# Performance work log

Hardware: AMD Instinct MI355X
Metric: run time of the kernel (lower is better)

## Reference

```python
import jax, jax.numpy as jnp
import numpy as np

EMBED_DIM = 1024
NUM_HEADS = 16
HEAD_WIDTH = 64  # EMBED_DIM == NUM_HEADS * HEAD_WIDTH
B, L = 2, 1024


def setup_inputs() -> dict:
    key = jax.random.key(0)
    ks = jax.random.split(key, 7)
    s = EMBED_DIM ** -0.5
    return {
        "x": jax.random.normal(ks[0], (B, L, EMBED_DIM), dtype=jnp.float32),
        "bias": jax.random.normal(ks[1], (B, L, L, NUM_HEADS), dtype=jnp.float32),
        # nn.Linear weights are (out_features, in_features)
        "w_proj": jax.random.normal(ks[2], (3 * EMBED_DIM, EMBED_DIM), dtype=jnp.float32) * s,
        "w_o": jax.random.normal(ks[3], (EMBED_DIM, EMBED_DIM), dtype=jnp.float32) * s,
        "b_o": jnp.zeros((EMBED_DIM,), dtype=jnp.float32),
        "w_g": jax.random.normal(ks[4], (EMBED_DIM, EMBED_DIM), dtype=jnp.float32) * s,
        "b_g": jnp.ones((EMBED_DIM,), dtype=jnp.float32),
    }


def reference(x, bias, w_proj, w_o, b_o, w_g, b_g):
    b, l, e = x.shape
    h, hw = NUM_HEADS, HEAD_WIDTH
    # fused QKV projection: (B,L,3E) -> (B,H,L,3*hw), head-major split as in torch
    t = jnp.einsum('ble,fe->blf', x, w_proj)
    t = t.reshape(b, l, h, 3 * hw).transpose(0, 2, 1, 3)  # (B,H,L,3hw)
    q, k, v = jnp.split(t, 3, axis=-1)
    q = q * (hw ** -0.5)
    a = jnp.einsum('bhqc,bhkc->bhqk', q, k)
    a = a + bias.transpose(0, 3, 1, 2)  # bias: (B,Lq,Lk,H) -> (B,H,Lq,Lk)
    a = jax.nn.softmax(a, axis=-1)
    y = jnp.einsum('bhqk,bhkc->bqhc', a, v).reshape(b, l, e)
    g = jax.nn.sigmoid(jnp.einsum('ble,fe->blf', x, w_g) + b_g)
    y = g * y
    y = jnp.einsum('ble,fe->blf', y, w_o) + b_o
    # faithful to original rearrange('... lq lk h -> ... h lq lk') applied to (B,h,lq,lk):
    attn = jnp.transpose(a, (0, 3, 1, 2))  # (B, lk, h, lq)
    return y, attn
```

## Files before the change

kernel.cpp:

```cpp
#include <hip/hip_runtime.h>
#include <hip/hip_bf16.h>
#include <stdint.h>

typedef __attribute__((ext_vector_type(4))) float f32x4;
typedef __attribute__((ext_vector_type(8))) short short8;
typedef __attribute__((ext_vector_type(4))) unsigned short u16x4;
typedef unsigned short us;

#define DEV __device__ __forceinline__
#define MFMA16(a, b, c) __builtin_amdgcn_mfma_f32_16x16x32_bf16(a, b, c, 0, 0, 0)

DEV us f2b(float x) {
  union { float f; uint32_t u; } c; c.f = x;
  uint32_t r = (c.u + 0x7fffu + ((c.u >> 16) & 1u)) >> 16;
  return (us)r;
}
DEV float b2f(us x) {
  union { uint32_t u; float f; } c; c.u = ((uint32_t)x) << 16;
  return c.f;
}

DEV void gload_lds16(const void* g, void* l) {
  __builtin_amdgcn_global_load_lds((const __attribute__((address_space(1))) void*)g,
                                   (__attribute__((address_space(3))) void*)l, 16, 0, 0);
}

__global__ __launch_bounds__(256) void prep_k(
    const float* __restrict__ x, const float* __restrict__ wproj,
    const float* __restrict__ wg, const float* __restrict__ wo,
    us* __restrict__ Xbf, us* __restrict__ Wbf, us* __restrict__ Wobf) {
  int i = blockIdx.x * 256 + threadIdx.x;
  const float* src; us* dst;
  if (i < 524288)               { src = x     + (size_t)i * 4;                  dst = Xbf + (size_t)i * 4; }
  else if (i < 524288 + 786432) { int j = i - 524288;            src = wproj + (size_t)j * 4; dst = Wbf + (size_t)j * 4; }
  else if (i < 524288 + 786432 + 262144) { int j = i - (524288 + 786432); src = wg + (size_t)j * 4; dst = Wbf + 3145728 + (size_t)j * 4; }
  else                          { int j = i - (524288 + 786432 + 262144); src = wo + (size_t)j * 4; dst = Wobf + (size_t)j * 4; }
  f32x4 v = *(const f32x4*)src;
  u16x4 o; o.x = f2b(v.x); o.y = f2b(v.y); o.z = f2b(v.z); o.w = f2b(v.w);
  *(u16x4*)dst = o;
}

DEV void gemm_stage(char* sm, const us* A, const us* Bw,
                    int tileMrow, int tileNrow, int buf, int kt, int lane, int wid) {
  const char* gA = (const char*)A;
  const char* gB = (const char*)Bw;
#pragma unroll
  for (int i = 0; i < 2; ++i) {
    int c = wid * 2 + i;
    int off = c * 1024 + lane * 16;
    int r = off >> 6, cb = off & 63;
    gload_lds16(gA + ((size_t)(tileMrow + r) * 2048) + kt * 64 + cb, sm + buf * 8192 + c * 1024);
    gload_lds16(gB + ((size_t)(tileNrow + r) * 2048) + kt * 64 + cb, sm + 16384 + buf * 8192 + c * 1024);
  }
}

DEV void gemm_main(const us* A, const us* Bw,
                   int tileMrow, int tileNrow, f32x4 acc[4][4], char* sm) {
  int tid = threadIdx.x, lane = tid & 63, wid = tid >> 6;
  int wr = wid >> 1, wc = wid & 1;
  gemm_stage(sm, A, Bw, tileMrow, tileNrow, 0, 0, lane, wid);
  for (int kt = 0; kt < 32; ++kt) {
    __syncthreads();
    if (kt < 31) gemm_stage(sm, A, Bw, tileMrow, tileNrow, (kt + 1) & 1, kt + 1, lane, wid);
    int ab = (kt & 1) * 8192;
    int rb = (lane & 15) * 64 + ((lane >> 4) * 16);
    short8 af[4], bf[4];
#pragma unroll
    for (int mi = 0; mi < 4; ++mi)
      af[mi] = *(const short8*)(sm + ab + (wr * 64 + mi * 16) * 64 + rb);
#pragma unroll
    for (int ni = 0; ni < 4; ++ni)
      bf[ni] = *(const short8*)(sm + 16384 + ab + (wc * 64 + ni * 16) * 64 + rb);
#pragma unroll
    for (int mi = 0; mi < 4; ++mi)
#pragma unroll
      for (int ni = 0; ni < 4; ++ni)
        acc[mi][ni] = MFMA16(af[mi], bf[ni], acc[mi][ni]);
  }
}

__global__ __launch_bounds__(256) void gemm_qkvg_k(
    const us* __restrict__ Xbf, const us* __restrict__ Wbf,
    us* __restrict__ Qb, us* __restrict__ Kb, us* __restrict__ Vt,
    float* __restrict__ G, const float* __restrict__ bg) {
  __shared__ char sm[32768];
  int bid = blockIdx.x;
  int swz = (bid & 7) * 64 + (bid >> 3);
  int tileM = swz >> 5, tileN = swz & 31;
  f32x4 acc[4][4] = {};
  gemm_main(Xbf, Wbf, tileM * 128, tileN * 128, acc, sm);
  int lane = threadIdx.x & 63, wid = threadIdx.x >> 6;
  int wr = wid >> 1, wc = wid & 1;
#pragma unroll
  for (int mi = 0; mi < 4; ++mi)
#pragma unroll
    for (int ni = 0; ni < 4; ++ni)
#pragma unroll
      for (int j = 0; j < 4; ++j) {
        int row = tileM * 128 + wr * 64 + mi * 16 + ((lane >> 4) << 2) + j;
        int col = tileN * 128 + wc * 64 + ni * 16 + (lane & 15);
        float v = acc[mi][ni][j];
        int b = row >> 10, l = row & 1023;
        if (col < 3072) {
          int h = col / 192, r = col - h * 192;
          size_t base = ((size_t)(b * 16 + h) * 1024 + l) * 64;
          if (r < 64)        Qb[base + r] = f2b(v * 0.125f);
          else if (r < 128)  Kb[base + (r - 64)] = f2b(v);
          else               Vt[((size_t)(b * 16 + h) * 64 + (r - 128)) * 1024 + l] = f2b(v);
        } else {
          int e = col - 3072;
          float s = v + bg[e];
          G[(size_t)row * 1024 + e] = 1.f / (1.f + __expf(-s));
        }
      }
}

__global__ __launch_bounds__(512, 8) void qke_k(
    const us* __restrict__ Qb, const us* __restrict__ Kb,
    const float* __restrict__ bias, us* __restrict__ E,
    float* __restrict__ lpart) {
  __shared__ float bt[2][8][16][36];
  int tid = threadIdx.x, lane = tid & 63, w = tid >> 6;
  int la = lane & 15, lg = lane >> 4;
  int bid = blockIdx.x;
  int b = (bid & 7) >> 2, kc = bid & 3;
  int hg = (bid >> 3) & 1, qt = bid >> 4;
  int lq0 = qt * 16, lk00 = kc * 256;
  int h = hg * 8 + w;
  int hh = w;

  short8 qf[2];
  {
    size_t bh = (size_t)(b * 16 + h);
#pragma unroll
    for (int ks = 0; ks < 2; ++ks)
      qf[ks] = *(const short8*)(Qb + bh * 65536 + (size_t)(lq0 + la) * 64 + ks * 32 + lg * 8);
  }
  const us* Kh = Kb + (size_t)(b * 16 + h) * 65536;
  const float* bsrc = bias + ((size_t)b << 24) + ((size_t)lq0 << 14) + hg * 8;

#pragma unroll
  for (int i = 0; i < 2; ++i) {
    int f = tid + i * 512;
    int h4 = f & 1, lk = (f >> 1) & 31, q = f >> 6;
    f32x4 v = *(const f32x4*)(bsrc + ((size_t)q << 14) + ((size_t)(lk00 + lk) << 4) + h4 * 4);
#pragma unroll
    for (int e = 0; e < 4; ++e) {
      int hl = h4 * 4 + e;
      bt[0][hl][q][lk ^ (hl << 2)] = v[e];
    }
  }

  float lacc = 0.f;
#pragma unroll 1
  for (int sc = 0; sc < 8; ++sc) {
    __syncthreads();
    if (sc < 7) {
      int lkg2 = lk00 + (sc + 1) * 32;
      int nb = (sc + 1) & 1;
#pragma unroll
      for (int i = 0; i < 2; ++i) {
        int f = tid + i * 512;
        int h4 = f & 1, lk = (f >> 1) & 31, q = f >> 6;
        f32x4 v = *(const f32x4*)(bsrc + ((size_t)q << 14) + ((size_t)(lkg2 + lk) << 4) + h4 * 4);
#pragma unroll
        for (int e = 0; e < 4; ++e) {
          int hl = h4 * 4 + e;
          bt[nb][hl][q][lk ^ (hl << 2)] = v[e];
        }
      }
    }
    int cb = sc & 1;
    int lkg = lk00 + sc * 32;
#pragma unroll
    for (int fr = 0; fr < 2; ++fr) {
      const us* kr = Kh + (size_t)(lkg + fr * 16 + la) * 64 + lg * 8;
      short8 kf0 = *(const short8*)kr;
      short8 kf1 = *(const short8*)(kr + 32);
      int lkb = (fr * 16 + lg * 4) ^ (hh << 2);
      f32x4 a = *(const f32x4*)&bt[cb][hh][la][lkb];
      a = MFMA16(kf0, qf[0], a);
      a = MFMA16(kf1, qf[1], a);
      u16x4 ev;
#pragma unroll
      for (int j = 0; j < 4; ++j) {
        float e = __expf(a[j]);
        lacc += e;
        ev[j] = f2b(e);
      }
      *(u16x4*)(E + (((size_t)(b * 1024 + lq0 + la) * 16 + h) << 10) + lkg + fr * 16 + lg * 4) = ev;
    }
  }
  {
    float s = lacc;
    s += __shfl_xor(s, 16);
    s += __shfl_xor(s, 32);
    if (lg == 0) lpart[kc * 32768 + (b * 16 + h) * 1024 + lq0 + la] = s;
  }
}

__global__ __launch_bounds__(256) void pv_k(
    const us* __restrict__ E, const us* __restrict__ Vt,
    const float* __restrict__ lpart, const float* __restrict__ G,
    float* __restrict__ outa, us* __restrict__ Ybf) {
  __shared__ char sm[49792];
  float* lv = (float*)(sm + 49664);
  int tid = threadIdx.x, lane = tid & 63, w = tid >> 6;
  int la = lane & 15, lg = lane >> 4;
  int bid = blockIdx.x;
  int g = bid >> 8, qt = (bid >> 3) & 31, xx = bid & 7;
  int bh = g * 8 + xx;
  int b = bh >> 4, h = bh & 15;
  int qb = qt * 32;
  if (tid < 32) {
    int r = bh * 1024 + qb + tid;
    float s = lpart[r] + lpart[32768 + r] + lpart[65536 + r] + lpart[98304 + r];
    lv[tid] = 1.f / s;
  }
  __syncthreads();
  char* pb = sm + w * 4096;
  const us* Vh = Vt + (size_t)bh * 65536;
  f32x4 yacc[2][4] = {};
  int lkw = w * 256;

#pragma unroll 1
  for (int cc = 0; cc < 4; ++cc) {
    int lk0 = lkw + cc * 64;
#pragma unroll
    for (int it = 0; it < 4; ++it) {
      int ci = it * 64 + lane;
      int q = ci >> 3, c16 = ci & 7;
      short8 ev = *(const short8*)(E + (((size_t)(b * 1024 + qb + q) * 16 + h) << 10) + lk0 + c16 * 8);
      *(short8*)(pb + q * 128 + ((c16 * 16) ^ ((q & 7) << 4))) = ev;
    }
#pragma unroll
    for (int it = 0; it < 8; ++it) {
      int idx = it * 64 + lane;
      int lkL = idx >> 3, q4 = idx & 7;
      f32x4 ov;
#pragma unroll
      for (int i = 0; i < 4; ++i) {
        int q = q4 * 4 + i;
        us e = *(const us*)(pb + q * 128 + ((2 * lkL) ^ ((q & 7) << 4)));
        ov[i] = b2f(e) * lv[q];
      }
      *(f32x4*)(outa + (((size_t)(b * 1024 + lk0 + lkL) * 16 + h) << 10) + qb + q4 * 4) = ov;
    }
#pragma unroll
    for (int ks = 0; ks < 2; ++ks) {
      short8 pa[2];
#pragma unroll
      for (int qh = 0; qh < 2; ++qh) {
        int row = qh * 16 + la;
        pa[qh] = *(const short8*)(pb + row * 128 + ((ks * 64 + lg * 16) ^ ((row & 7) << 4)));
      }
#pragma unroll
      for (int ni = 0; ni < 4; ++ni) {
        short8 vf = *(const short8*)(Vh + (size_t)(ni * 16 + la) * 1024 + lk0 + ks * 32 + lg * 8);
        yacc[0][ni] = MFMA16(pa[0], vf, yacc[0][ni]);
        yacc[1][ni] = MFMA16(pa[1], vf, yacc[1][ni]);
      }
    }
  }

  float* red = (float*)(sm + 16384);
#pragma unroll
  for (int qh = 0; qh < 2; ++qh)
#pragma unroll
    for (int ni = 0; ni < 4; ++ni)
#pragma unroll
      for (int j = 0; j < 4; ++j) {
        int r = qh * 16 + lg * 4 + j, c = ni * 16 + la;
        red[w * 2080 + r * 65 + c] = yacc[qh][ni][j];
      }
  __syncthreads();
#pragma unroll
  for (int rr = 0; rr < 8; ++rr) {
    int e = rr * 256 + tid;
    int r = e >> 6, c = e & 63;
    float s = red[r * 65 + c] + red[2080 + r * 65 + c] +
              red[4160 + r * 65 + c] + red[6240 + r * 65 + c];
    size_t gi = (((size_t)(b * 1024 + qb + r)) << 10) + h * 64 + c;
    Ybf[gi] = f2b(s * lv[r] * G[gi]);
  }
}

__global__ __launch_bounds__(256) void gemm_out_k(
    const us* __restrict__ Ybf, const us* __restrict__ Wobf,
    const float* __restrict__ bo, float* __restrict__ outy) {
  __shared__ char sm[32768];
  int bid = blockIdx.x;
  int swz = (bid & 7) * 16 + (bid >> 3);
  int tileM = swz >> 3, tileN = swz & 7;
  f32x4 acc[4][4] = {};
  gemm_main(Ybf, Wobf, tileM * 128, tileN * 128, acc, sm);
  int lane = threadIdx.x & 63, wid = threadIdx.x >> 6;
  int wr = wid >> 1, wc = wid & 1;
#pragma unroll
  for (int mi = 0; mi < 4; ++mi)
#pragma unroll
    for (int ni = 0; ni < 4; ++ni)
#pragma unroll
      for (int j = 0; j < 4; ++j) {
        int row = tileM * 128 + wr * 64 + mi * 16 + ((lane >> 4) << 2) + j;
        int col = tileN * 128 + wc * 64 + ni * 16 + (lane & 15);
        outy[(size_t)row * 1024 + col] = acc[mi][ni][j] + bo[col];
      }
}

extern "C" void kernel_launch(void* const* d_in, const int* in_sizes, int n_in,
                              void* d_out, int out_size, void* d_ws, size_t ws_size,
                              hipStream_t stream) {
  const float* x     = (const float*)d_in[0];
  const float* bias  = (const float*)d_in[1];
  const float* wproj = (const float*)d_in[2];
  const float* wo    = (const float*)d_in[3];
  const float* bo    = (const float*)d_in[4];
  const float* wg    = (const float*)d_in[5];
  const float* bg    = (const float*)d_in[6];
  float* outy = (float*)d_out;
  float* outa = outy + 2097152;

  char* ws = (char*)d_ws;
  us*    Xbf  = (us*)(ws);
  us*    Wbf  = (us*)(ws + 4  * 1024 * 1024);
  us*    Wobf = (us*)(ws + 12 * 1024 * 1024);
  us*    Qb   = (us*)(ws + 14 * 1024 * 1024);
  us*    Kb   = (us*)(ws + 18 * 1024 * 1024);
  us*    Vt   = (us*)(ws + 22 * 1024 * 1024);
  float* G    = (float*)(ws + 26 * 1024 * 1024);
  us*    Ybf  = (us*)(ws + 34 * 1024 * 1024);
  float* lpart= (float*)(ws + (size_t)38 * 1024 * 1024);
  us*    E    = (us*)   (ws + (size_t)40 * 1024 * 1024);
  if (ws_size < (size_t)104 * 1024 * 1024) return;

  prep_k<<<dim3(7168), dim3(256), 0, stream>>>(x, wproj, wg, wo, Xbf, Wbf, Wobf);
  gemm_qkvg_k<<<dim3(512), dim3(256), 0, stream>>>(Xbf, Wbf, Qb, Kb, Vt, G, bg);
  qke_k<<<dim3(1024), dim3(512), 0, stream>>>(Qb, Kb, bias, E, lpart);
  pv_k<<<dim3(1024), dim3(256), 0, stream>>>(E, Vt, lpart, G, outa, Ybf);
  gemm_out_k<<<dim3(128), dim3(256), 0, stream>>>(Ybf, Wobf, bo, outy);
}
```

Measured before the change: 200.5 us.

## Restructure qke bias staging into two large 128-key phases with register prefetch

The qke kernel's 8-step double-buffered loop, which loaded 32 keys of bias per step with a barrier each time, becomes two phases of 128 keys. Each phase issues 8 vector loads per thread into registers. The second half's bias loads are issued before the first half's MFMA/exp work, so the global latency overlaps compute, and only two barriers remain. The cost is a 4x larger LDS buffer (about 147KB) and more registers, so launch bounds drop to 4 waves per SIMD and occupancy falls.

```diff
diff --git a/kernel.cpp b/kernel.cpp
--- a/kernel.cpp
+++ b/kernel.cpp
@@ -115,19 +115,18 @@
       }
 }
 
-__global__ __launch_bounds__(512, 8) void qke_k(
+__global__ __launch_bounds__(512, 4) void qke_k(
     const us* __restrict__ Qb, const us* __restrict__ Kb,
     const float* __restrict__ bias, us* __restrict__ E,
     float* __restrict__ lpart) {
-  __shared__ float bt[2][8][16][36];
+  __shared__ float bt[2][4][8][16][36];
   int tid = threadIdx.x, lane = tid & 63, w = tid >> 6;
   int la = lane & 15, lg = lane >> 4;
   int bid = blockIdx.x;
   int b = (bid & 7) >> 2, kc = bid & 3;
   int hg = (bid >> 3) & 1, qt = bid >> 4;
   int lq0 = qt * 16, lk00 = kc * 256;
-  int h = hg * 8 + w;
-  int hh = w;
+  int h = hg * 8 + w, hh = w;
 
   short8 qf[2];
   {
@@ -138,58 +137,84 @@
   }
   const us* Kh = Kb + (size_t)(b * 16 + h) * 65536;
   const float* bsrc = bias + ((size_t)b << 24) + ((size_t)lq0 << 14) + hg * 8;
-
-#pragma unroll
-  for (int i = 0; i < 2; ++i) {
-    int f = tid + i * 512;
-    int h4 = f & 1, lk = (f >> 1) & 31, q = f >> 6;
-    f32x4 v = *(const f32x4*)(bsrc + ((size_t)q << 14) + ((size_t)(lk00 + lk) << 4) + h4 * 4);
+  us* Erow = E + (((size_t)(b * 1024 + lq0 + la) * 16 + h) << 10);
+
+  f32x4 vv[8];
+#pragma unroll
+  for (int i = 0; i < 8; ++i) {
+    int f = i * 512 + tid;
+    int h4 = f & 1, lk = (f >> 1) & 127, q = f >> 8;
+    vv[i] = *(const f32x4*)(bsrc + ((size_t)q << 14) + ((size_t)(lk00 + lk) << 4) + h4 * 4);
+  }
+#pragma unroll
+  for (int i = 0; i < 8; ++i) {
+    int f = i * 512 + tid;
+    int h4 = f & 1, lk = (f >> 1) & 127, q = f >> 8;
+    int c = lk >> 5, slk = lk & 31;
 #pragma unroll
     for (int e = 0; e < 4; ++e) {
       int hl = h4 * 4 + e;
-      bt[0][hl][q][lk ^ (hl << 2)] = v[e];
-    }
-  }
+      bt[0][c][hl][q][slk ^ (hl << 2)] = vv[i][e];
+    }
+  }
+  __syncthreads();
 
   float lacc = 0.f;
-#pragma unroll 1
-  for (int sc = 0; sc < 8; ++sc) {
-    __syncthreads();
-    if (sc < 7) {
-      int lkg2 = lk00 + (sc + 1) * 32;
-      int nb = (sc + 1) & 1;
-#pragma unroll
-      for (int i = 0; i < 2; ++i) {
-        int f = tid + i * 512;
-        int h4 = f & 1, lk = (f >> 1) & 31, q = f >> 6;
-        f32x4 v = *(const f32x4*)(bsrc + ((size_t)q << 14) + ((size_t)(lkg2 + lk) << 4) + h4 * 4);
-#pragma unroll
-        for (int e = 0; e < 4; ++e) {
-          int hl = h4 * 4 + e;
-          bt[nb][hl][q][lk ^ (hl << 2)] = v[e];
-        }
-      }
-    }
-    int cb = sc & 1;
-    int lkg = lk00 + sc * 32;
-#pragma unroll
-    for (int fr = 0; fr < 2; ++fr) {
-      const us* kr = Kh + (size_t)(lkg + fr * 16 + la) * 64 + lg * 8;
-      short8 kf0 = *(const short8*)kr;
-      short8 kf1 = *(const short8*)(kr + 32);
-      int lkb = (fr * 16 + lg * 4) ^ (hh << 2);
-      f32x4 a = *(const f32x4*)&bt[cb][hh][la][lkb];
-      a = MFMA16(kf0, qf[0], a);
-      a = MFMA16(kf1, qf[1], a);
-      u16x4 ev;
-#pragma unroll
-      for (int j = 0; j < 4; ++j) {
-        float e = __expf(a[j]);
-        lacc += e;
-        ev[j] = f2b(e);
-      }
-      *(u16x4*)(E + (((size_t)(b * 1024 + lq0 + la) * 16 + h) << 10) + lkg + fr * 16 + lg * 4) = ev;
-    }
+#pragma unroll
+  for (int i = 0; i < 8; ++i) {
+    int f = i * 512 + tid;
+    int h4 = f & 1, lk = (f >> 1) & 127, q = f >> 8;
+    vv[i] = *(const f32x4*)(bsrc + ((size_t)q << 14) + ((size_t)(lk00 + 128 + lk) << 4) + h4 * 4);
+  }
+#pragma unroll
+  for (int fr = 0; fr < 8; ++fr) {
+    int c = fr >> 1;
+    const us* kr = Kh + (size_t)(lk00 + fr * 16 + la) * 64 + lg * 8;
+    short8 kf0 = *(const short8*)kr;
+    short8 kf1 = *(const short8*)(kr + 32);
+    int lkb = ((fr & 1) * 16 + lg * 4) ^ (hh << 2);
+    f32x4 a = *(const f32x4*)&bt[0][c][hh][la][lkb];
+    a = MFMA16(kf0, qf[0], a);
+    a = MFMA16(kf1, qf[1], a);
+    u16x4 ev;
+#pragma unroll
+    for (int j = 0; j < 4; ++j) {
+      float e = __expf(a[j]);
+      lacc += e;
+      ev[j] = f2b(e);
+    }
+    *(u16x4*)(Erow + lk00 + fr * 16 + lg * 4) = ev;
+  }
+#pragma unroll
+  for (int i = 0; i < 8; ++i) {
+    int f = i * 512 + tid;
+    int h4 = f & 1, lk = (f >> 1) & 127, q = f >> 8;
+    int c = lk >> 5, slk = lk & 31;
+#pragma unroll
+    for (int e = 0; e < 4; ++e) {
+      int hl = h4 * 4 + e;
+      bt[1][c][hl][q][slk ^ (hl << 2)] = vv[i][e];
+    }
+  }
+  __syncthreads();
+#pragma unroll
+  for (int fr = 0; fr < 8; ++fr) {
+    int c = fr >> 1;
+    const us* kr = Kh + (size_t)(lk00 + 128 + fr * 16 + la) * 64 + lg * 8;
+    short8 kf0 = *(const short8*)kr;
+    short8 kf1 = *(const short8*)(kr + 32);
+    int lkb = ((fr & 1) * 16 + lg * 4) ^ (hh << 2);
+    f32x4 a = *(const f32x4*)&bt[1][c][hh][la][lkb];
+    a = MFMA16(kf0, qf[0], a);
+    a = MFMA16(kf1, qf[1], a);
+    u16x4 ev;
+#pragma unroll
+    for (int j = 0; j < 4; ++j) {
+      float e = __expf(a[j]);
+      lacc += e;
+      ev[j] = f2b(e);
+    }
+    *(u16x4*)(Erow + lk00 + 128 + fr * 16 + lg * 4) = ev;
   }
   {
     float s = lacc;
```

Result: faster. 195.1 us, median of 3 (-2.7%).
